# Performance work log

Measured on AMD Instinct MI355X. Metric: run time of the kernel, lower is better.

## Reference

```python
import jax, jax.numpy as jnp
import numpy as np

B, S, F_IN, D, H, L, E, DFF, OUT = 16, 512, 46, 256, 8, 6, 8, 1024, 3


def _ln(x, s, b, eps=1e-5):
    m = x.mean(-1, keepdims=True)
    v = ((x - m) ** 2).mean(-1, keepdims=True)
    return (x - m) / jnp.sqrt(v + eps) * s + b


def _mha(q_in, kv_in, qkv_w, qkv_b, out_w, out_b, h):
    # torch nn.MultiheadAttention (batch_first), eval mode (no dropout)
    d = q_in.shape[-1]
    dh = d // h
    wq, wk, wv = jnp.split(qkv_w, 3, axis=0)
    bq, bk, bv = jnp.split(qkv_b, 3)
    q = (q_in @ wq.T + bq).reshape(q_in.shape[0], q_in.shape[1], h, dh)
    k = (kv_in @ wk.T + bk).reshape(kv_in.shape[0], kv_in.shape[1], h, dh)
    v = (kv_in @ wv.T + bv).reshape(kv_in.shape[0], kv_in.shape[1], h, dh)
    attn = jax.nn.softmax(jnp.einsum('bqhd,bkhd->bhqk', q, k) / jnp.sqrt(jnp.float32(dh)), axis=-1)
    o = jnp.einsum('bhqk,bkhd->bqhd', attn, v).reshape(q_in.shape[0], q_in.shape[1], d)
    return o @ out_w.T + out_b


def _moe(x, gate_w, gate_b, e_w1, e_b1, e_w2, e_b2, top_k=2):
    # Faithful to source: EVERY expert runs its dense FFN over all tokens,
    # then outputs are mixed by the top-k gate weights (zero for unrouted experts).
    logits = x @ gate_w.T + gate_b                      # (B,S,E)
    tk_logits, tk_idx = jax.lax.top_k(logits, top_k)    # (B,S,K)
    tk_probs = jax.nn.softmax(tk_logits, axis=-1)
    onehot = jax.nn.one_hot(tk_idx, logits.shape[-1], dtype=x.dtype)  # (B,S,K,E)
    weights = (onehot * tk_probs[..., None]).sum(-2)    # (B,S,E)
    hid = jax.nn.gelu(jnp.einsum('bsd,efd->bsef', x, e_w1) + e_b1, approximate=False)  # (B,S,E,DFF)
    out_e = jnp.einsum('bsef,edf->bsed', hid, e_w2) + e_b2                             # (B,S,E,D)
    out = jnp.einsum('bsed,bse->bsd', out_e, weights)
    probs = jax.nn.softmax(logits, axis=-1)
    aux = logits.shape[-1] * jnp.sum(probs.mean(axis=(0, 1)) ** 2)
    return out, aux


def _posenc(s, d):
    pos = jnp.arange(s, dtype=jnp.float32)[:, None]
    div = jnp.exp(jnp.arange(0, d, 2, dtype=jnp.float32) * (-np.log(10000.0) / d))
    pe = jnp.zeros((s, d), jnp.float32)
    pe = pe.at[:, 0::2].set(jnp.sin(pos * div)).at[:, 1::2].set(jnp.cos(pos * div))
    return pe


def _forward(x, in_w, in_b, l_qkv_w, l_qkv_b, l_out_w, l_out_b, gate_w, gate_b,
             e_w1, e_b1, e_w2, e_b2, ln1_s, ln1_b, ln2_s, ln2_b,
             p_qkv_w, p_qkv_b, p_out_w, p_out_b,
             a_w1, a_b1, a_ln1s, a_ln1b, a_w2, a_b2, a_ln2s, a_ln2b, a_w3, a_b3,
             pr_w1, pr_b1, pr_ln1s, pr_ln1b, pr_w2, pr_b2, pr_ln2s, pr_ln2b, pr_w3, pr_b3):
    h = x @ in_w.T + in_b + _posenc(x.shape[1], D)[None]
    aux_total = jnp.float32(0.0)
    # NB: source builds ModuleList([encoder_layer]*L) with the SAME instance -> shared weights
    for _ in range(L):
        attn = _mha(h, h, l_qkv_w, l_qkv_b, l_out_w, l_out_b, H)
        h = _ln(h + attn, ln1_s, ln1_b)
        moe_out, aux = _moe(h, gate_w, gate_b, e_w1, e_b1, e_w2, e_b2)
        aux_total = aux_total + aux
        h = _ln(h + moe_out, ln2_s, ln2_b)
    pooled = _mha(h[:, -1:, :], h, p_qkv_w, p_qkv_b, p_out_w, p_out_b, H)[:, 0]  # (B,D)
    # action head: Linear -> GELU -> LN -> Linear -> GELU -> LN -> Linear
    a = jax.nn.gelu(pooled @ a_w1.T + a_b1, approximate=False)
    a = _ln(a, a_ln1s, a_ln1b)
    a = jax.nn.gelu(a @ a_w2.T + a_b2, approximate=False)
    a = _ln(a, a_ln2s, a_ln2b)
    action = a @ a_w3.T + a_b3
    # profit head: Linear -> LN -> GELU -> Linear -> LN -> GELU -> Linear
    p = jax.nn.gelu(_ln(pooled @ pr_w1.T + pr_b1, pr_ln1s, pr_ln1b), approximate=False)
    p = jax.nn.gelu(_ln(p @ pr_w2.T + pr_b2, pr_ln2s, pr_ln2b), approximate=False)
    profit = p @ pr_w3.T + pr_b3
    return action, profit, aux_total


def setup_inputs() -> dict:
    key = jax.random.key(0)
    ks = iter(jax.random.split(key, 64))
    def w(shape, scale=0.02):
        return jax.random.normal(next(ks), shape, jnp.float32) * scale
    d2, d4 = D // 2, D // 4
    return dict(
        x=jax.random.normal(next(ks), (B, S, F_IN), jnp.float32),
        in_w=w((D, F_IN)), in_b=jnp.zeros(D),
        l_qkv_w=w((3 * D, D)), l_qkv_b=jnp.zeros(3 * D), l_out_w=w((D, D)), l_out_b=jnp.zeros(D),
        gate_w=w((E, D)), gate_b=jnp.zeros(E),
        e_w1=w((E, DFF, D)), e_b1=jnp.zeros((E, DFF)), e_w2=w((E, D, DFF)), e_b2=jnp.zeros((E, D)),
        ln1_s=jnp.ones(D), ln1_b=jnp.zeros(D), ln2_s=jnp.ones(D), ln2_b=jnp.zeros(D),
        p_qkv_w=w((3 * D, D)), p_qkv_b=jnp.zeros(3 * D), p_out_w=w((D, D)), p_out_b=jnp.zeros(D),
        a_w1=w((d2, D)), a_b1=jnp.zeros(d2), a_ln1s=jnp.ones(d2), a_ln1b=jnp.zeros(d2),
        a_w2=w((d4, d2)), a_b2=jnp.zeros(d4), a_ln2s=jnp.ones(d4), a_ln2b=jnp.zeros(d4),
        a_w3=w((OUT, d4)), a_b3=jnp.zeros(OUT),
        pr_w1=w((D, D)), pr_b1=jnp.zeros(D), pr_ln1s=jnp.ones(D), pr_ln1b=jnp.zeros(D),
        pr_w2=w((d2, D)), pr_b2=jnp.zeros(d2), pr_ln2s=jnp.ones(d2), pr_ln2b=jnp.zeros(d2),
        pr_w3=w((1, d2)), pr_b3=jnp.zeros(1),
    )


def reference(x, in_w, in_b, l_qkv_w, l_qkv_b, l_out_w, l_out_b, gate_w, gate_b,
              e_w1, e_b1, e_w2, e_b2, ln1_s, ln1_b, ln2_s, ln2_b,
              p_qkv_w, p_qkv_b, p_out_w, p_out_b,
              a_w1, a_b1, a_ln1s, a_ln1b, a_w2, a_b2, a_ln2s, a_ln2b, a_w3, a_b3,
              pr_w1, pr_b1, pr_ln1s, pr_ln1b, pr_w2, pr_b2, pr_ln2s, pr_ln2b, pr_w3, pr_b3):
    return _forward(x, in_w, in_b, l_qkv_w, l_qkv_b, l_out_w, l_out_b, gate_w, gate_b,
                    e_w1, e_b1, e_w2, e_b2, ln1_s, ln1_b, ln2_s, ln2_b,
                    p_qkv_w, p_qkv_b, p_out_w, p_out_b,
                    a_w1, a_b1, a_ln1s, a_ln1b, a_w2, a_b2, a_ln2s, a_ln2b, a_w3, a_b3,
                    pr_w1, pr_b1, pr_ln1s, pr_ln1b, pr_w2, pr_b2, pr_ln2s, pr_ln2b, pr_w3, pr_b3)
```

## Files before the change

### kernel.cpp

```cpp
#include <hip/hip_runtime.h>
#include <hip/hip_bf16.h>
#include <math.h>


typedef __bf16 bf16;
typedef __bf16 bf16x8 __attribute__((ext_vector_type(8)));
typedef __bf16 bf16x4 __attribute__((ext_vector_type(4)));
typedef float f32x4 __attribute__((ext_vector_type(4)));

#define NIN 41

#define GLOAD_LDS(g, l)                                                    \
    __builtin_amdgcn_global_load_lds(                                      \
        (const __attribute__((address_space(1))) void*)(g),                \
        (__attribute__((address_space(3))) void*)(l), 16, 0, 0)

struct InTab {
    const void* src[NIN];
    unsigned off[NIN];
    unsigned n[NIN];
};

__device__ __forceinline__ float gelu_exact(float x) {
    return 0.5f * x * (1.0f + erff(x * 0.70710678118654752f));
}

__device__ __forceinline__ float gelu_fast(float x) {
    const float u = fabsf(x) * 0.70710678118654752f;
    const float t = 1.0f / (1.0f + 0.3275911f * u);
    const float p = t * (0.254829592f + t * (-0.284496736f + t * (1.421413741f +
                    t * (-1.453152027f + t * 1.061405429f))));
    const float er = 1.0f - p * __builtin_exp2f(-u * u * 1.4426950408889634f);
    const float s = (x >= 0.0f) ? er : -er;
    return 0.5f * x * (1.0f + s);
}

__global__ void sniff_kernel(const unsigned* __restrict__ xw, int* __restrict__ flag) {
    __shared__ int cnt;
    if (threadIdx.x == 0) cnt = 0;
    __syncthreads();
    const unsigned w = xw[threadIdx.x];
    const unsigned ex = (w >> 7) & 0xFFu;
    if (ex >= 107u && ex <= 133u) atomicAdd(&cnt, 1);
    __syncthreads();
    if (threadIdx.x == 0) *flag = (cnt >= 192) ? 1 : 0;
}

__global__ __launch_bounds__(256) void convert_kernel(
    InTab tab, bf16* __restrict__ dst_base, const int* __restrict__ flag) {
    const unsigned g0 = blockIdx.x * 1024u;
    int inp = 0;
#pragma unroll
    for (int i = 1; i < NIN; i++)
        if (g0 >= tab.off[i]) inp = i;
    const unsigned n = tab.n[inp];
    const unsigned i0 = g0 - tab.off[inp] + threadIdx.x * 4u;
    if (i0 >= n) return;
    const int isbf = *flag;
    bf16* dst = dst_base + tab.off[inp];
    const unsigned end = (i0 + 4u > n) ? n : i0 + 4u;
    if (isbf) {
        const unsigned short* s = (const unsigned short*)tab.src[inp];
        for (unsigned i = i0; i < end; i++) ((unsigned short*)dst)[i] = s[i];
    } else {
        const float* s = (const float*)tab.src[inp];
        for (unsigned i = i0; i < end; i++) dst[i] = (bf16)s[i];
    }
}

__global__ void out_convert_kernel(const float* __restrict__ st,
                                   const float* __restrict__ auxsums,
                                   void* __restrict__ out,
                                   const int* __restrict__ flag) {
    const int i = threadIdx.x;
    if (i >= 65) return;
    float v;
    if (i == 64) {
        float tot = 0.0f;
        for (int l = 0; l < 6; l++)
            for (int e = 0; e < 8; e++) {
                const float mn = auxsums[l * 8 + e] * (1.0f / 8192.0f);
                tot += 8.0f * mn * mn;
            }
        v = tot;
    } else {
        v = st[i];
    }
    if (*flag) ((bf16*)out)[i] = (bf16)v;
    else       ((float*)out)[i] = v;
}

#define SWZ(r, c) (((r) * 8 + ((c) ^ ((r) & 7))) * 8)

template <int BM, int BN, int WM, int WN, bool VTOUT>
__global__ __launch_bounds__(256) void gemm_bt(
    const bf16* __restrict__ A, const bf16* __restrict__ W,
    const bf16* __restrict__ bias, bf16* __restrict__ C,
    int M, int N, int K, bf16* __restrict__ vT) {
    constexpr int BK = 64;
    __shared__ alignas(16) bf16 smem[BM * BK + BN * BK];
    bf16* As = smem;
    bf16* Ws = smem + BM * BK;
    const int bm0 = blockIdx.x * BM, bn0 = blockIdx.y * BN;
    const int tid = threadIdx.x;
    const int wave = tid >> 6, lane = tid & 63;
    constexpr int WCOLS = BN / WN;
    const int wm0 = (wave / WCOLS) * WM, wn0 = (wave % WCOLS) * WN;
    constexpr int MT = WM / 16, NT = WN / 16;
    f32x4 acc[MT][NT] = {};
    const int frow = lane & 15, fquad = lane >> 4;

    constexpr int AIT = BM / 32, BIT = BN / 32;
    const bf16* ag[AIT];
    const bf16* bg[BIT];
    unsigned al[AIT], bl[BIT];
#pragma unroll
    for (int i = 0; i < AIT; i++) {
        const int d = wave * (BM * 2) + i * 64 + lane;
        const int r = d >> 3, c = ((d & 7) ^ (r & 7)) * 8;
        ag[i] = A + (size_t)(bm0 + r) * K + c;
        al[i] = (unsigned)(wave * (BM * 2) + i * 64) * 8u;
    }
#pragma unroll
    for (int i = 0; i < BIT; i++) {
        const int d = wave * (BN * 2) + i * 64 + lane;
        const int r = d >> 3, c = ((d & 7) ^ (r & 7)) * 8;
        bg[i] = W + (size_t)(bn0 + r) * K + c;
        bl[i] = (unsigned)(wave * (BN * 2) + i * 64) * 8u;
    }

    for (int k0 = 0; k0 < K; k0 += BK) {
#pragma unroll
        for (int i = 0; i < AIT; i++) GLOAD_LDS(ag[i] + k0, &As[al[i]]);
#pragma unroll
        for (int i = 0; i < BIT; i++) GLOAD_LDS(bg[i] + k0, &Ws[bl[i]]);
        __syncthreads();
#pragma unroll
        for (int ks = 0; ks < BK / 32; ks++) {
            bf16x8 af[MT], bfr[NT];
#pragma unroll
            for (int mt = 0; mt < MT; mt++) {
                const int r = wm0 + mt * 16 + frow;
                af[mt] = *(const bf16x8*)&As[SWZ(r, ks * 4 + fquad)];
            }
#pragma unroll
            for (int nt = 0; nt < NT; nt++) {
                const int r = wn0 + nt * 16 + frow;
                bfr[nt] = *(const bf16x8*)&Ws[SWZ(r, ks * 4 + fquad)];
            }
#pragma unroll
            for (int mt = 0; mt < MT; mt++)
#pragma unroll
                for (int nt = 0; nt < NT; nt++)
                    acc[mt][nt] = __builtin_amdgcn_mfma_f32_16x16x32_bf16(
                        af[mt], bfr[nt], acc[mt][nt], 0, 0, 0);
        }
        __syncthreads();
    }

    if (VTOUT && bn0 >= 512) {
#pragma unroll
        for (int mt = 0; mt < MT; mt++)
#pragma unroll
            for (int nt = 0; nt < NT; nt++) {
                const int gn = bn0 + wn0 + nt * 16 + frow;
                const float bv = (float)bias[gn];
                bf16x4 o4;
#pragma unroll
                for (int r = 0; r < 4; r++) o4[r] = (bf16)(acc[mt][nt][r] + bv);
                const int gm0 = bm0 + wm0 + mt * 16 + fquad * 4;
                const int d = gn - 512;
                *(bf16x4*)&vT[((size_t)((gm0 >> 9) * 8 + (d >> 5)) * 32 + (d & 31)) * 512 +
                              (gm0 & 511)] = o4;
            }
    } else {
        bf16* Cs = smem;
#pragma unroll
        for (int mt = 0; mt < MT; mt++)
#pragma unroll
            for (int nt = 0; nt < NT; nt++) {
                const int cl = wn0 + nt * 16 + frow;
                const float bv = (float)bias[bn0 + cl];
#pragma unroll
                for (int r = 0; r < 4; r++)
                    Cs[(wm0 + mt * 16 + fquad * 4 + r) * BN + cl] =
                        (bf16)(acc[mt][nt][r] + bv);
            }
        __syncthreads();
        constexpr int CPR = BN / 8;
        constexpr int CH = (BM * BN) / (256 * 8);
#pragma unroll
        for (int i = 0; i < CH; i++) {
            const int ch = tid + i * 256;
            const int row = ch / CPR;
            const int col = (ch % CPR) * 8;
            *(bf16x8*)&C[(size_t)(bm0 + row) * N + bn0 + col] =
                *(const bf16x8*)&Cs[row * BN + col];
        }
    }
}

__global__ __launch_bounds__(256) void gemm_moe_w1(
    const bf16* __restrict__ A, const bf16* __restrict__ Wb,
    const bf16* __restrict__ biasb, bf16* __restrict__ hid0,
    bf16* __restrict__ hid1, const int* __restrict__ list,
    const int* __restrict__ tile_ex, const int* __restrict__ ntiles) {
    constexpr int BM = 128, BN = 128, BK = 64, WM = 64, WN = 64;
    constexpr int N = 1024, K = 256;
    const int slot = (blockIdx.x >= 71) ? 1 : 0;
    const int xi = blockIdx.x - slot * 71;
    if (xi >= ntiles[slot]) return;
    __shared__ alignas(16) bf16 smem[BM * BK + BN * BK];
    bf16* As = smem;
    bf16* Ws = smem + BM * BK;
    const int* mylist = list + slot * 9216;
    const int e = tile_ex[slot * 72 + xi];
    const bf16* W = Wb + (size_t)e * N * K;
    const bf16* bias = biasb + e * N;
    bf16* C = slot ? hid1 : hid0;
    const int bm0 = xi * BM, bn0 = blockIdx.y * BN;
    const int tid = threadIdx.x;
    const int wave = tid >> 6, lane = tid & 63;
    constexpr int WCOLS = BN / WN;
    const int wm0 = (wave / WCOLS) * WM, wn0 = (wave % WCOLS) * WN;
    constexpr int MT = WM / 16, NT = WN / 16;
    f32x4 acc[MT][NT] = {};
    const int frow = lane & 15, fquad = lane >> 4;

    const bf16* ag[4];
    const bf16* bg[4];
    unsigned al[4], bl[4];
#pragma unroll
    for (int i = 0; i < 4; i++) {
        const int d = wave * 256 + i * 64 + lane;
        const int r = d >> 3, c = ((d & 7) ^ (r & 7)) * 8;
        ag[i] = A + (size_t)mylist[bm0 + r] * K + c;
        al[i] = (unsigned)(wave * 256 + i * 64) * 8u;
        bg[i] = W + (size_t)(bn0 + r) * K + c;
        bl[i] = al[i];
    }

    for (int k0 = 0; k0 < K; k0 += BK) {
#pragma unroll
        for (int i = 0; i < 4; i++) GLOAD_LDS(ag[i] + k0, &As[al[i]]);
#pragma unroll
        for (int i = 0; i < 4; i++) GLOAD_LDS(bg[i] + k0, &Ws[bl[i]]);
        __syncthreads();
#pragma unroll
        for (int ks = 0; ks < 2; ks++) {
            bf16x8 af[MT], bfr[NT];
#pragma unroll
            for (int mt = 0; mt < MT; mt++) {
                const int r = wm0 + mt * 16 + frow;
                af[mt] = *(const bf16x8*)&As[SWZ(r, ks * 4 + fquad)];
            }
#pragma unroll
            for (int nt = 0; nt < NT; nt++) {
                const int r = wn0 + nt * 16 + frow;
                bfr[nt] = *(const bf16x8*)&Ws[SWZ(r, ks * 4 + fquad)];
            }
#pragma unroll
            for (int mt = 0; mt < MT; mt++)
#pragma unroll
                for (int nt = 0; nt < NT; nt++)
                    acc[mt][nt] = __builtin_amdgcn_mfma_f32_16x16x32_bf16(
                        af[mt], bfr[nt], acc[mt][nt], 0, 0, 0);
        }
        __syncthreads();
    }

    {
        bf16* Cs = smem;
#pragma unroll
        for (int mt = 0; mt < MT; mt++)
#pragma unroll
            for (int nt = 0; nt < NT; nt++) {
                const int cl = wn0 + nt * 16 + frow;
                const float bv = (float)bias[bn0 + cl];
#pragma unroll
                for (int r = 0; r < 4; r++)
                    Cs[(wm0 + mt * 16 + fquad * 4 + r) * BN + cl] =
                        (bf16)gelu_fast(acc[mt][nt][r] + bv);
            }
        __syncthreads();
#pragma unroll
        for (int i = 0; i < 8; i++) {
            const int ch = tid + i * 256;
            const int row = ch >> 4;
            const int col = (ch & 15) * 8;
            *(bf16x8*)&C[(size_t)(bm0 + row) * N + bn0 + col] =
                *(const bf16x8*)&Cs[row * BN + col];
        }
    }
}

__global__ __launch_bounds__(256) void gemm_moe_w2(
    const bf16* __restrict__ hid0, const bf16* __restrict__ hid1,
    const bf16* __restrict__ Wb, const bf16* __restrict__ biasb,
    bf16* __restrict__ moe0, bf16* __restrict__ moe1,
    const int* __restrict__ list, const float* __restrict__ lw,
    const int* __restrict__ tile_ex, const int* __restrict__ ntiles) {
    constexpr int BM = 128, BN = 64, BK = 64, WM = 32;
    constexpr int N = 256, K = 1024;
    const int slot = (blockIdx.x >= 71) ? 1 : 0;
    const int xi = blockIdx.x - slot * 71;
    if (xi >= ntiles[slot]) return;
    __shared__ alignas(16) bf16 smem[BM * BK + BN * BK];
    bf16* As = smem;
    bf16* Ws = smem + BM * BK;
    const bf16* A = slot ? hid1 : hid0;
    bf16* C = slot ? moe1 : moe0;
    const int* mylist = list + slot * 9216;
    const float* mylw = lw + slot * 9216;
    const int e = tile_ex[slot * 72 + xi];
    const bf16* W = Wb + (size_t)e * N * K;
    const bf16* bias = biasb + e * N;
    const int bm0 = xi * BM, bn0 = blockIdx.y * BN;
    const int tid = threadIdx.x;
    const int wave = tid >> 6, lane = tid & 63;
    const int wm0 = wave * WM;
    constexpr int MT = WM / 16, NT = 4;
    f32x4 acc[MT][NT] = {};
    const int frow = lane & 15, fquad = lane >> 4;

    const bf16* ag[4];
    const bf16* bg[2];
    unsigned al[4], bl[2];
#pragma unroll
    for (int i = 0; i < 4; i++) {
        const int d = wave * 256 + i * 64 + lane;
        const int r = d >> 3, c = ((d & 7) ^ (r & 7)) * 8;
        ag[i] = A + (size_t)(bm0 + r) * K + c;
        al[i] = (unsigned)(wave * 256 + i * 64) * 8u;
    }
#pragma unroll
    for (int i = 0; i < 2; i++) {
        const int d = wave * 128 + i * 64 + lane;
        const int r = d >> 3, c = ((d & 7) ^ (r & 7)) * 8;
        bg[i] = W + (size_t)(bn0 + r) * K + c;
        bl[i] = (unsigned)(wave * 128 + i * 64) * 8u;
    }

    for (int k0 = 0; k0 < K; k0 += BK) {
#pragma unroll
        for (int i = 0; i < 4; i++) GLOAD_LDS(ag[i] + k0, &As[al[i]]);
#pragma unroll
        for (int i = 0; i < 2; i++) GLOAD_LDS(bg[i] + k0, &Ws[bl[i]]);
        __syncthreads();
#pragma unroll
        for (int ks = 0; ks < 2; ks++) {
            bf16x8 af[MT], bfr[NT];
#pragma unroll
            for (int mt = 0; mt < MT; mt++) {
                const int r = wm0 + mt * 16 + frow;
                af[mt] = *(const bf16x8*)&As[SWZ(r, ks * 4 + fquad)];
            }
#pragma unroll
            for (int nt = 0; nt < NT; nt++) {
                const int r = nt * 16 + frow;
                bfr[nt] = *(const bf16x8*)&Ws[SWZ(r, ks * 4 + fquad)];
            }
#pragma unroll
            for (int mt = 0; mt < MT; mt++)
#pragma unroll
                for (int nt = 0; nt < NT; nt++)
                    acc[mt][nt] = __builtin_amdgcn_mfma_f32_16x16x32_bf16(
                        af[mt], bfr[nt], acc[mt][nt], 0, 0, 0);
        }
        __syncthreads();
    }

    {
        bf16* Cs = smem;
        float lwv[MT][4];
#pragma unroll
        for (int mt = 0; mt < MT; mt++)
#pragma unroll
            for (int r = 0; r < 4; r++)
                lwv[mt][r] = mylw[bm0 + wm0 + mt * 16 + fquad * 4 + r];
#pragma unroll
        for (int mt = 0; mt < MT; mt++)
#pragma unroll
            for (int nt = 0; nt < NT; nt++) {
                const int cl = nt * 16 + frow;
                const float bv = (float)bias[bn0 + cl];
#pragma unroll
                for (int r = 0; r < 4; r++)
                    Cs[(wm0 + mt * 16 + fquad * 4 + r) * BN + cl] =
                        (bf16)(lwv[mt][r] * (acc[mt][nt][r] + bv));
            }
        __syncthreads();
#pragma unroll
        for (int i = 0; i < 4; i++) {
            const int ch = tid + i * 256;
            const int row = ch >> 3;
            const int col = (ch & 7) * 8;
            *(bf16x8*)&C[(size_t)mylist[bm0 + row] * 256 + bn0 + col] =
                *(const bf16x8*)&Cs[row * BN + col];
        }
    }
}

__global__ __launch_bounds__(256) void input_proj_kernel(
    const bf16* __restrict__ x, const bf16* __restrict__ w,
    const bf16* __restrict__ b, bf16* __restrict__ h) {
    const int m = blockIdx.x, t = threadIdx.x;
    __shared__ float xs[46];
    if (t < 46) xs[t] = (float)x[m * 46 + t];
    __syncthreads();
    float acc = (float)b[t];
#pragma unroll
    for (int k = 0; k < 46; k++) acc += xs[k] * (float)w[t * 46 + k];
    const int s = m & 511;
    const int i = t >> 1;
    const float dv = expf((float)(2 * i) * (-9.210340371976184f / 256.0f));
    const float ang = (float)s * dv;
    const float pe = (t & 1) ? cosf(ang) : sinf(ang);
    h[(size_t)m * 256 + t] = (bf16)(acc + pe);
}

__global__ __launch_bounds__(256) void ln_kernel(
    bf16* __restrict__ h, const bf16* __restrict__ a0,
    const bf16* __restrict__ a1, const bf16* __restrict__ s,
    const bf16* __restrict__ b) {
    const int wv = threadIdx.x >> 6, lane = threadIdx.x & 63;
    const int m = blockIdx.x * 8 + wv * 2 + (lane >> 5);
    const int c0 = (lane & 31) * 8;
    const size_t off = (size_t)m * 256 + c0;
    bf16x8 hv = *(const bf16x8*)&h[off];
    bf16x8 av = *(const bf16x8*)&a0[off];
    bf16x8 bv2 = *(const bf16x8*)&a1[off];
    float x[8];
    float s1 = 0.0f, s2 = 0.0f;
#pragma unroll
    for (int j = 0; j < 8; j++) {
        x[j] = (float)hv[j] + (float)av[j] + (float)bv2[j];
        s1 += x[j];
        s2 += x[j] * x[j];
    }
#pragma unroll
    for (int msk = 1; msk < 32; msk <<= 1) {
        s1 += __shfl_xor(s1, msk, 64);
        s2 += __shfl_xor(s2, msk, 64);
    }
    const float mean = s1 * (1.0f / 256.0f);
    const float var = fmaxf(s2 * (1.0f / 256.0f) - mean * mean, 0.0f);
    const float inv = rsqrtf(var + 1e-5f);
    bf16x8 sv = *(const bf16x8*)&s[c0];
    bf16x8 bv = *(const bf16x8*)&b[c0];
    bf16x8 o;
#pragma unroll
    for (int j = 0; j < 8; j++)
        o[j] = (bf16)((x[j] - mean) * inv * (float)sv[j] + (float)bv[j]);
    *(bf16x8*)&h[off] = o;
}

__global__ __launch_bounds__(256) void proj_gate_ln_kernel(
    const bf16* __restrict__ A, const bf16* __restrict__ W,
    const bf16* __restrict__ bias, bf16* __restrict__ h,
    const bf16* __restrict__ lns, const bf16* __restrict__ lnb,
    const bf16* __restrict__ gw, const bf16* __restrict__ gb,
    int* __restrict__ top_e, float* __restrict__ top_w,
    int* __restrict__ g_hist, float* __restrict__ aux_sums) {
    __shared__ alignas(16) bf16 As[32 * 64];
    __shared__ alignas(16) bf16 Ws[256 * 64];
    __shared__ alignas(16) bf16 hs[32 * 264];
    __shared__ alignas(16) bf16 gws[8 * 264];
    __shared__ float rws1[4][32], rws2[4][32];
    __shared__ float meanv[32], invv[32];
    __shared__ float lg[256];
    __shared__ int sh_hist[16];
    __shared__ float sh_aux[8];

    const int bm0 = blockIdx.x * 32;
    const int tid = threadIdx.x;
    const int wave = tid >> 6, lane = tid & 63;
    const int wn0 = (wave & 3) * 64;
    const int frow = lane & 15, fquad = lane >> 4;
    f32x4 acc[2][4] = {};

    const int da = wave * 64 + lane;
// ... 429 lines not shown
        for (int k = 0; k < 256; k += 8) {
            bf16x8 wv = *(const bf16x8*)&wr[k];
#pragma unroll
            for (int q = 0; q < 8; q++) a += pool[k + q] * (float)wv[q];
        }
        buf[t] = gelu_exact(a);
    }
    __syncthreads();
    block_ln(buf, 128, aln1s, aln1b);
    if (t < 64) {
        float a = (float)ab2[t];
        const bf16* wr = &aw2[t * 128];
        for (int k = 0; k < 128; k += 8) {
            bf16x8 wv = *(const bf16x8*)&wr[k];
#pragma unroll
            for (int q = 0; q < 8; q++) a += buf[k + q] * (float)wv[q];
        }
        buf2[t] = gelu_exact(a);
    }
    __syncthreads();
    block_ln(buf2, 64, aln2s, aln2b);
    if (t < 3) {
        float a = (float)ab3[t];
        for (int k = 0; k < 64; k++) a += buf2[k] * (float)aw3[t * 64 + k];
        out[b * 3 + t] = a;
    }

    {
        float a = (float)pb1[t];
        const bf16* wr = &pw1[t * 256];
        for (int k = 0; k < 256; k += 8) {
            bf16x8 wv = *(const bf16x8*)&wr[k];
#pragma unroll
            for (int q = 0; q < 8; q++) a += pool[k + q] * (float)wv[q];
        }
        buf[t] = a;
    }
    __syncthreads();
    block_ln(buf, 256, pln1s, pln1b);
    buf[t] = gelu_exact(buf[t]);
    __syncthreads();
    if (t < 128) {
        float a = (float)pb2[t];
        const bf16* wr = &pw2[t * 256];
        for (int k = 0; k < 256; k += 8) {
            bf16x8 wv = *(const bf16x8*)&wr[k];
#pragma unroll
            for (int q = 0; q < 8; q++) a += buf[k + q] * (float)wv[q];
        }
        buf2[t] = a;
    }
    __syncthreads();
    block_ln(buf2, 128, pln2s, pln2b);
    if (t < 128) buf2[t] = gelu_exact(buf2[t]);
    __syncthreads();
    if (t == 0) {
        float a = (float)pb3[0];
        for (int k = 0; k < 128; k++) a += buf2[k] * (float)pw3[k];
        out[48 + b] = a;
    }
}

extern "C" void kernel_launch(void* const* d_in, const int* in_sizes, int n_in,
                              void* d_out, int out_size, void* d_ws, size_t ws_size,
                              hipStream_t stream) {
    char* ws = (char*)d_ws;
    const size_t MB = 1024 * 1024;
    bf16*  h     = (bf16*)(ws);
    bf16*  moe0  = (bf16*)(ws + 8 * MB);
    bf16*  moe1  = (bf16*)(ws + 13 * MB);
    char*  ctrl  = ws + 20 * MB;
    float* auxs   = (float*)(ctrl + 0);
    int*   flag   = (int*)(ctrl + 192);
    int*   ntiles = (int*)(ctrl + 256);
    int*   tileex = (int*)(ctrl + 320);
    float* ostage = (float*)(ctrl + 1024);
    int*   g_hist = (int*)(ctrl + 2048);
    int*   top_e  = (int*)(ctrl + 20480);
    float* top_w  = (float*)(ctrl + 86016);
    int*   list   = (int*)(ctrl + 151552);
    float* lw     = (float*)(ctrl + 225280);
    bf16*  qkv   = (bf16*)(ws + 24 * MB);
    bf16*  aoutb = (bf16*)(ws + 40 * MB);
    bf16*  hid0  = (bf16*)(ws + 56 * MB);
    bf16*  hid1  = (bf16*)(ws + 80 * MB);
    bf16*  vT    = (bf16*)(ws + 104 * MB);
    float* pattn = (float*)(ws + 110 * MB);
    bf16*  cvbase = (bf16*)(ws + 112 * MB);

    InTab tab;
    unsigned off = 0;
    bf16* cv[NIN];
    for (int i = 0; i < NIN; i++) {
        tab.src[i] = d_in[i];
        tab.off[i] = off;
        tab.n[i] = (unsigned)in_sizes[i];
        cv[i] = cvbase + off;
        off += ((unsigned)in_sizes[i] + 1023u) & ~1023u;
    }
    const int cv_blocks = (int)(off >> 10);

    const bf16 *x = cv[0], *in_w = cv[1], *in_b = cv[2], *qkv_w = cv[3], *qkv_b = cv[4],
               *out_w = cv[5], *out_b = cv[6], *gate_w = cv[7], *gate_b = cv[8],
               *e_w1 = cv[9], *e_b1 = cv[10], *e_w2 = cv[11], *e_b2 = cv[12],
               *ln1_s = cv[13], *ln1_b = cv[14], *ln2_s = cv[15], *ln2_b = cv[16],
               *pqkv_w = cv[17], *pqkv_b = cv[18], *pout_w = cv[19], *pout_b = cv[20],
               *a_w1 = cv[21], *a_b1 = cv[22], *a_ln1s = cv[23], *a_ln1b = cv[24],
               *a_w2 = cv[25], *a_b2 = cv[26], *a_ln2s = cv[27], *a_ln2b = cv[28],
               *a_w3 = cv[29], *a_b3 = cv[30],
               *pr_w1 = cv[31], *pr_b1 = cv[32], *pr_ln1s = cv[33], *pr_ln1b = cv[34],
               *pr_w2 = cv[35], *pr_b2 = cv[36], *pr_ln2s = cv[37], *pr_ln2b = cv[38],
               *pr_w3 = cv[39], *pr_b3 = cv[40];

    sniff_kernel<<<1, 256, 0, stream>>>((const unsigned*)d_in[0], flag);
    convert_kernel<<<cv_blocks, 256, 0, stream>>>(tab, cvbase, flag);

    hipMemsetAsync(auxs, 0, 192, stream);
    input_proj_kernel<<<8192, 256, 0, stream>>>(x, in_w, in_b, h);

    for (int l = 0; l < 6; l++) {
        gemm_bt<64, 128, 32, 64, true><<<dim3(128, 6), 256, 0, stream>>>(
            h, qkv_w, qkv_b, qkv, 8192, 768, 256, vT);
        attn_kernel<<<dim3(16, 128), 256, 0, stream>>>(qkv, vT, aoutb);
        proj_gate_ln_kernel<<<256, 256, 0, stream>>>(
            aoutb, out_w, out_b, h, ln1_s, ln1_b, gate_w, gate_b,
            top_e, top_w, g_hist, auxs + l * 8);
        scatter_route_kernel<<<64, 256, 0, stream>>>(g_hist, top_e, top_w,
                                                     ntiles, tileex, list, lw);
        gemm_moe_w1<<<dim3(142, 8), 256, 0, stream>>>(
            h, e_w1, e_b1, hid0, hid1, list, tileex, ntiles);
        gemm_moe_w2<<<dim3(142, 4), 256, 0, stream>>>(
            hid0, hid1, e_w2, e_b2, moe0, moe1, list, lw, tileex, ntiles);
        ln_kernel<<<1024, 256, 0, stream>>>(h, moe0, moe1, ln2_s, ln2_b);
    }

    gemm_bt<64, 128, 32, 64, true><<<dim3(128, 6), 256, 0, stream>>>(
        h, pqkv_w, pqkv_b, qkv, 8192, 768, 256, vT);
    pooled_attn_kernel<<<128, 256, 0, stream>>>(qkv, vT, pattn);
    heads_kernel<<<16, 256, 0, stream>>>(
        pattn, pout_w, pout_b,
        a_w1, a_b1, a_ln1s, a_ln1b, a_w2, a_b2, a_ln2s, a_ln2b, a_w3, a_b3,
        pr_w1, pr_b1, pr_ln1s, pr_ln1b, pr_w2, pr_b2, pr_ln2s, pr_ln2b, pr_w3, pr_b3,
        ostage);
    out_convert_kernel<<<1, 128, 0, stream>>>(ostage, auxs, d_out, flag);
}
```

Measured before the change: 1.007 ms.

## Fuse MoE expert W1+GELU and W2 GEMMs into one kernel keeping hidden in LDS

Replaces the two routed-expert GEMM kernels with a single fused kernel. Each block takes 32 routed tokens, computes the hidden activations in 256-column chunks into shared memory, and immediately accumulates the second GEMM. This avoids writing and re-reading the large hidden tensor through global memory and drops one launch. The cost is smaller M tiles with low per-block reuse of expert weights, each block re-reading the full W1/W2 for its expert, and no load/compute overlap. It also zeroes a padding row after h, presumably to cover a sentinel index in the gather lists.

```diff
diff --git a/kernel.cpp b/kernel.cpp
--- a/kernel.cpp
+++ b/kernel.cpp
@@ -91,6 +91,7 @@
 }
 
 #define SWZ(r, c) (((r) * 8 + ((c) ^ ((r) & 7))) * 8)
+#define SWZ256(r, c) (((r) * 32 + ((c) ^ ((r) & 7))) * 8)
 
 template <int BM, int BN, int WM, int WN, bool VTOUT>
 __global__ __launch_bounds__(256) void gemm_bt(
@@ -200,203 +201,147 @@
     }
 }
 
-__global__ __launch_bounds__(256) void gemm_moe_w1(
-    const bf16* __restrict__ A, const bf16* __restrict__ Wb,
-    const bf16* __restrict__ biasb, bf16* __restrict__ hid0,
-    bf16* __restrict__ hid1, const int* __restrict__ list,
-    const int* __restrict__ tile_ex, const int* __restrict__ ntiles) {
-    constexpr int BM = 128, BN = 128, BK = 64, WM = 64, WN = 64;
-    constexpr int N = 1024, K = 256;
-    const int slot = (blockIdx.x >= 71) ? 1 : 0;
-    const int xi = blockIdx.x - slot * 71;
-    if (xi >= ntiles[slot]) return;
-    __shared__ alignas(16) bf16 smem[BM * BK + BN * BK];
-    bf16* As = smem;
-    bf16* Ws = smem + BM * BK;
+__global__ __launch_bounds__(256) void gemm_moe_fused(
+    const bf16* __restrict__ hsrc, const bf16* __restrict__ W1b,
+    const bf16* __restrict__ b1b, const bf16* __restrict__ W2b,
+    const bf16* __restrict__ b2b, bf16* __restrict__ moe0,
+    bf16* __restrict__ moe1, const int* __restrict__ list,
+    const float* __restrict__ lw, const int* __restrict__ tile_ex,
+    const int* __restrict__ ntiles) {
+    __shared__ alignas(16) bf16 As[32 * 256];
+    __shared__ alignas(16) bf16 Hs[32 * 256];
+    __shared__ alignas(16) bf16 Ws[256 * 64];
+    const int slot = (blockIdx.x >= 284) ? 1 : 0;
+    const int xi = (int)blockIdx.x - slot * 284;
+    if (xi >= (ntiles[slot] << 2)) return;
     const int* mylist = list + slot * 9216;
-    const int e = tile_ex[slot * 72 + xi];
-    const bf16* W = Wb + (size_t)e * N * K;
-    const bf16* bias = biasb + e * N;
-    bf16* C = slot ? hid1 : hid0;
-    const int bm0 = xi * BM, bn0 = blockIdx.y * BN;
-    const int tid = threadIdx.x;
-    const int wave = tid >> 6, lane = tid & 63;
-    constexpr int WCOLS = BN / WN;
-    const int wm0 = (wave / WCOLS) * WM, wn0 = (wave % WCOLS) * WN;
-    constexpr int MT = WM / 16, NT = WN / 16;
-    f32x4 acc[MT][NT] = {};
+    const float* mylw = lw + slot * 9216;
+    const int e = tile_ex[slot * 72 + (xi >> 2)];
+    const bf16* W1 = W1b + (size_t)e * 1024 * 256;
+    const bf16* b1 = b1b + e * 1024;
+    const bf16* W2 = W2b + (size_t)e * 256 * 1024;
+    const bf16* b2 = b2b + e * 256;
+    bf16* C = slot ? moe1 : moe0;
+    const int bm0 = xi * 32;
+    const int tid = threadIdx.x, wave = tid >> 6, lane = tid & 63;
     const int frow = lane & 15, fquad = lane >> 4;
-
-    const bf16* ag[4];
-    const bf16* bg[4];
-    unsigned al[4], bl[4];
+    const int wn0 = wave * 64;
+
 #pragma unroll
     for (int i = 0; i < 4; i++) {
         const int d = wave * 256 + i * 64 + lane;
-        const int r = d >> 3, c = ((d & 7) ^ (r & 7)) * 8;
-        ag[i] = A + (size_t)mylist[bm0 + r] * K + c;
-        al[i] = (unsigned)(wave * 256 + i * 64) * 8u;
-        bg[i] = W + (size_t)(bn0 + r) * K + c;
-        bl[i] = al[i];
-    }
-
-    for (int k0 = 0; k0 < K; k0 += BK) {
-#pragma unroll
-        for (int i = 0; i < 4; i++) GLOAD_LDS(ag[i] + k0, &As[al[i]]);
-#pragma unroll
-        for (int i = 0; i < 4; i++) GLOAD_LDS(bg[i] + k0, &Ws[bl[i]]);
-        __syncthreads();
-#pragma unroll
-        for (int ks = 0; ks < 2; ks++) {
-            bf16x8 af[MT], bfr[NT];
-#pragma unroll
-            for (int mt = 0; mt < MT; mt++) {
-                const int r = wm0 + mt * 16 + frow;
-                af[mt] = *(const bf16x8*)&As[SWZ(r, ks * 4 + fquad)];
-            }
-#pragma unroll
-            for (int nt = 0; nt < NT; nt++) {
-                const int r = wn0 + nt * 16 + frow;
-                bfr[nt] = *(const bf16x8*)&Ws[SWZ(r, ks * 4 + fquad)];
-            }
-#pragma unroll
-            for (int mt = 0; mt < MT; mt++)
-#pragma unroll
-                for (int nt = 0; nt < NT; nt++)
-                    acc[mt][nt] = __builtin_amdgcn_mfma_f32_16x16x32_bf16(
-                        af[mt], bfr[nt], acc[mt][nt], 0, 0, 0);
-        }
-        __syncthreads();
+        const int r = d >> 5, c = ((d & 31) ^ (r & 7)) * 8;
+        GLOAD_LDS(hsrc + (size_t)mylist[bm0 + r] * 256 + c, &As[d * 8]);
+    }
+
+    f32x4 macc[2][4] = {};
+#pragma unroll 1
+    for (int nc = 0; nc < 4; nc++) {
+        f32x4 acc1[2][4] = {};
+        for (int k0 = 0; k0 < 256; k0 += 64) {
+#pragma unroll
+            for (int i = 0; i < 8; i++) {
+                const int d = wave * 512 + i * 64 + lane;
+                const int r = d >> 3, c = ((d & 7) ^ (r & 7)) * 8;
+                GLOAD_LDS(W1 + (size_t)(nc * 256 + r) * 256 + k0 + c, &Ws[d * 8]);
+            }
+            __syncthreads();
+#pragma unroll
+            for (int ks = 0; ks < 2; ks++) {
+                bf16x8 af[2], bfr[4];
+#pragma unroll
+                for (int mt = 0; mt < 2; mt++) {
+                    const int r = mt * 16 + frow;
+                    const int kc = (k0 >> 3) + ks * 4 + fquad;
+                    af[mt] = *(const bf16x8*)&As[SWZ256(r, kc)];
+                }
+#pragma unroll
+                for (int nt = 0; nt < 4; nt++) {
+                    const int r = wn0 + nt * 16 + frow;
+                    bfr[nt] = *(const bf16x8*)&Ws[SWZ(r, ks * 4 + fquad)];
+                }
+#pragma unroll
+                for (int mt = 0; mt < 2; mt++)
+#pragma unroll
+                    for (int nt = 0; nt < 4; nt++)
+                        acc1[mt][nt] = __builtin_amdgcn_mfma_f32_16x16x32_bf16(
+                            af[mt], bfr[nt], acc1[mt][nt], 0, 0, 0);
+            }
+            __syncthreads();
+        }
+#pragma unroll
+        for (int mt = 0; mt < 2; mt++)
+#pragma unroll
+            for (int nt = 0; nt < 4; nt++) {
+                const int gn = wn0 + nt * 16 + frow;
+                const float bv = (float)b1[nc * 256 + gn];
+#pragma unroll
+                for (int r = 0; r < 4; r++) {
+                    const int gm = mt * 16 + fquad * 4 + r;
+                    Hs[SWZ256(gm, gn >> 3) + (gn & 7)] =
+                        (bf16)gelu_fast(acc1[mt][nt][r] + bv);
+                }
+            }
+        __syncthreads();
+        for (int k0 = 0; k0 < 256; k0 += 64) {
+#pragma unroll
+            for (int i = 0; i < 8; i++) {
+                const int d = wave * 512 + i * 64 + lane;
+                const int r = d >> 3, c = ((d & 7) ^ (r & 7)) * 8;
+                GLOAD_LDS(W2 + (size_t)r * 1024 + nc * 256 + k0 + c, &Ws[d * 8]);
+            }
+            __syncthreads();
+#pragma unroll
+            for (int ks = 0; ks < 2; ks++) {
+                bf16x8 af[2], bfr[4];
+#pragma unroll
+                for (int mt = 0; mt < 2; mt++) {
+                    const int r = mt * 16 + frow;
+                    const int kc = (k0 >> 3) + ks * 4 + fquad;
+                    af[mt] = *(const bf16x8*)&Hs[SWZ256(r, kc)];
+                }
+#pragma unroll
+                for (int nt = 0; nt < 4; nt++) {
+                    const int r = wn0 + nt * 16 + frow;
+                    bfr[nt] = *(const bf16x8*)&Ws[SWZ(r, ks * 4 + fquad)];
+                }
+#pragma unroll
+                for (int mt = 0; mt < 2; mt++)
+#pragma unroll
+                    for (int nt = 0; nt < 4; nt++)
+                        macc[mt][nt] = __builtin_amdgcn_mfma_f32_16x16x32_bf16(
+                            af[mt], bfr[nt], macc[mt][nt], 0, 0, 0);
+            }
+            __syncthreads();
+        }
     }
 
     {
-        bf16* Cs = smem;
-#pragma unroll
-        for (int mt = 0; mt < MT; mt++)
-#pragma unroll
-            for (int nt = 0; nt < NT; nt++) {
-                const int cl = wn0 + nt * 16 + frow;
-                const float bv = (float)bias[bn0 + cl];
-#pragma unroll
-                for (int r = 0; r < 4; r++)
-                    Cs[(wm0 + mt * 16 + fquad * 4 + r) * BN + cl] =
-                        (bf16)gelu_fast(acc[mt][nt][r] + bv);
-            }
-        __syncthreads();
-#pragma unroll
-        for (int i = 0; i < 8; i++) {
-            const int ch = tid + i * 256;
-            const int row = ch >> 4;
-            const int col = (ch & 15) * 8;
-            *(bf16x8*)&C[(size_t)(bm0 + row) * N + bn0 + col] =
-                *(const bf16x8*)&Cs[row * BN + col];
-        }
-    }
-}
-
-__global__ __launch_bounds__(256) void gemm_moe_w2(
-    const bf16* __restrict__ hid0, const bf16* __restrict__ hid1,
-    const bf16* __restrict__ Wb, const bf16* __restrict__ biasb,
-    bf16* __restrict__ moe0, bf16* __restrict__ moe1,
-    const int* __restrict__ list, const float* __restrict__ lw,
-    const int* __restrict__ tile_ex, const int* __restrict__ ntiles) {
-    constexpr int BM = 128, BN = 64, BK = 64, WM = 32;
-    constexpr int N = 256, K = 1024;
-    const int slot = (blockIdx.x >= 71) ? 1 : 0;
-    const int xi = blockIdx.x - slot * 71;
-    if (xi >= ntiles[slot]) return;
-    __shared__ alignas(16) bf16 smem[BM * BK + BN * BK];
-    bf16* As = smem;
-    bf16* Ws = smem + BM * BK;
-    const bf16* A = slot ? hid1 : hid0;
-    bf16* C = slot ? moe1 : moe0;
-    const int* mylist = list + slot * 9216;
-    const float* mylw = lw + slot * 9216;
-    const int e = tile_ex[slot * 72 + xi];
-    const bf16* W = Wb + (size_t)e * N * K;
-    const bf16* bias = biasb + e * N;
-    const int bm0 = xi * BM, bn0 = blockIdx.y * BN;
-    const int tid = threadIdx.x;
-    const int wave = tid >> 6, lane = tid & 63;
-    const int wm0 = wave * WM;
-    constexpr int MT = WM / 16, NT = 4;
-    f32x4 acc[MT][NT] = {};
-    const int frow = lane & 15, fquad = lane >> 4;
-
-    const bf16* ag[4];
-    const bf16* bg[2];
-    unsigned al[4], bl[2];
-#pragma unroll
-    for (int i = 0; i < 4; i++) {
-        const int d = wave * 256 + i * 64 + lane;
-        const int r = d >> 3, c = ((d & 7) ^ (r & 7)) * 8;
-        ag[i] = A + (size_t)(bm0 + r) * K + c;
-        al[i] = (unsigned)(wave * 256 + i * 64) * 8u;
-    }
-#pragma unroll
-    for (int i = 0; i < 2; i++) {
-        const int d = wave * 128 + i * 64 + lane;
-        const int r = d >> 3, c = ((d & 7) ^ (r & 7)) * 8;
-        bg[i] = W + (size_t)(bn0 + r) * K + c;
-        bl[i] = (unsigned)(wave * 128 + i * 64) * 8u;
-    }
-
-    for (int k0 = 0; k0 < K; k0 += BK) {
-#pragma unroll
-        for (int i = 0; i < 4; i++) GLOAD_LDS(ag[i] + k0, &As[al[i]]);
-#pragma unroll
-        for (int i = 0; i < 2; i++) GLOAD_LDS(bg[i] + k0, &Ws[bl[i]]);
-        __syncthreads();
-#pragma unroll
-        for (int ks = 0; ks < 2; ks++) {
-            bf16x8 af[MT], bfr[NT];
-#pragma unroll
-            for (int mt = 0; mt < MT; mt++) {
-                const int r = wm0 + mt * 16 + frow;
-                af[mt] = *(const bf16x8*)&As[SWZ(r, ks * 4 + fquad)];
-            }
-#pragma unroll
-            for (int nt = 0; nt < NT; nt++) {
-                const int r = nt * 16 + frow;
-                bfr[nt] = *(const bf16x8*)&Ws[SWZ(r, ks * 4 + fquad)];
-            }
-#pragma unroll
-            for (int mt = 0; mt < MT; mt++)
-#pragma unroll
-                for (int nt = 0; nt < NT; nt++)
-                    acc[mt][nt] = __builtin_amdgcn_mfma_f32_16x16x32_bf16(
-                        af[mt], bfr[nt], acc[mt][nt], 0, 0, 0);
-        }
-        __syncthreads();
-    }
-
-    {
-        bf16* Cs = smem;
-        float lwv[MT][4];
-#pragma unroll
-        for (int mt = 0; mt < MT; mt++)
+        float lwv[2][4];
+#pragma unroll
+        for (int mt = 0; mt < 2; mt++)
 #pragma unroll
             for (int r = 0; r < 4; r++)
-                lwv[mt][r] = mylw[bm0 + wm0 + mt * 16 + fquad * 4 + r];
-#pragma unroll
-        for (int mt = 0; mt < MT; mt++)
-#pragma unroll
-            for (int nt = 0; nt < NT; nt++) {
-                const int cl = nt * 16 + frow;
-                const float bv = (float)bias[bn0 + cl];
-#pragma unroll
-                for (int r = 0; r < 4; r++)
-                    Cs[(wm0 + mt * 16 + fquad * 4 + r) * BN + cl] =
-                        (bf16)(lwv[mt][r] * (acc[mt][nt][r] + bv));
+                lwv[mt][r] = mylw[bm0 + mt * 16 + fquad * 4 + r];
+#pragma unroll
+        for (int mt = 0; mt < 2; mt++)
+#pragma unroll
+            for (int nt = 0; nt < 4; nt++) {
+                const int gn = wn0 + nt * 16 + frow;
+                const float bv = (float)b2[gn];
+#pragma unroll
+                for (int r = 0; r < 4; r++) {
+                    const int gm = mt * 16 + fquad * 4 + r;
+                    As[gm * 256 + gn] = (bf16)(lwv[mt][r] * (macc[mt][nt][r] + bv));
+                }
             }
         __syncthreads();
 #pragma unroll
         for (int i = 0; i < 4; i++) {
             const int ch = tid + i * 256;
-            const int row = ch >> 3;
-            const int col = (ch & 7) * 8;
-            *(bf16x8*)&C[(size_t)mylist[bm0 + row] * 256 + bn0 + col] =
-                *(const bf16x8*)&Cs[row * BN + col];
+            const int row = ch >> 5, col = (ch & 31) * 8;
+            *(bf16x8*)&C[(size_t)mylist[bm0 + row] * 256 + col] =
+                *(const bf16x8*)&As[row * 256 + col];
         }
     }
 }
@@ -992,8 +937,6 @@
     float* lw     = (float*)(ctrl + 225280);
     bf16*  qkv   = (bf16*)(ws + 24 * MB);
     bf16*  aoutb = (bf16*)(ws + 40 * MB);
-    bf16*  hid0  = (bf16*)(ws + 56 * MB);
-    bf16*  hid1  = (bf16*)(ws + 80 * MB);
     bf16*  vT    = (bf16*)(ws + 104 * MB);
     float* pattn = (float*)(ws + 110 * MB);
     bf16*  cvbase = (bf16*)(ws + 112 * MB);
@@ -1026,6 +969,7 @@
     convert_kernel<<<cv_blocks, 256, 0, stream>>>(tab, cvbase, flag);
 
     hipMemsetAsync(auxs, 0, 192, stream);
+    hipMemsetAsync((char*)h + (size_t)8192 * 512, 0, 512, stream);
     input_proj_kernel<<<8192, 256, 0, stream>>>(x, in_w, in_b, h);
 
     for (int l = 0; l < 6; l++) {
@@ -1037,10 +981,8 @@
             top_e, top_w, g_hist, auxs + l * 8);
         scatter_route_kernel<<<64, 256, 0, stream>>>(g_hist, top_e, top_w,
                                                      ntiles, tileex, list, lw);
-        gemm_moe_w1<<<dim3(142, 8), 256, 0, stream>>>(
-            h, e_w1, e_b1, hid0, hid1, list, tileex, ntiles);
-        gemm_moe_w2<<<dim3(142, 4), 256, 0, stream>>>(
-            hid0, hid1, e_w2, e_b2, moe0, moe1, list, lw, tileex, ntiles);
+        gemm_moe_fused<<<568, 256, 0, stream>>>(
+            h, e_w1, e_b1, e_w2, e_b2, moe0, moe1, list, lw, tileex, ntiles);
         ln_kernel<<<1024, 256, 0, stream>>>(h, moe0, moe1, ln2_s, ln2_b);
     }
 
```

Result: slower. 1.126 ms (+11.9%).

## Double-buffer LDS staging in MoE expert GEMMs to overlap loads with MFMA

Applied to the files above, without the earlier changes.

Both MoE expert GEMM kernels now use two LDS buffers per operand. The next K-slice is issued with global_load_lds before the current slice is computed, and explicit vmcnt waits plus raw barriers replace __syncthreads. The goal is to hide global-to-LDS latency behind the MFMA work instead of stalling every iteration. In exchange, shared-memory use per block doubles, which may lower occupancy, and correctness depends on the hand-set vmcnt counts matching the number of outstanding loads.

```diff
diff --git a/kernel.cpp b/kernel.cpp
--- a/kernel.cpp
+++ b/kernel.cpp
@@ -210,9 +210,8 @@
     const int slot = (blockIdx.x >= 71) ? 1 : 0;
     const int xi = blockIdx.x - slot * 71;
     if (xi >= ntiles[slot]) return;
-    __shared__ alignas(16) bf16 smem[BM * BK + BN * BK];
-    bf16* As = smem;
-    bf16* Ws = smem + BM * BK;
+    __shared__ alignas(16) bf16 As[2][BM * BK];
+    __shared__ alignas(16) bf16 Ws[2][BN * BK];
     const int* mylist = list + slot * 9216;
     const int e = tile_ex[slot * 72 + xi];
     const bf16* W = Wb + (size_t)e * N * K;
@@ -240,24 +239,36 @@
         bl[i] = al[i];
     }
 
+    auto stage = [&](int buf, int k0) {
+#pragma unroll
+        for (int i = 0; i < 4; i++) GLOAD_LDS(ag[i] + k0, &As[buf][al[i]]);
+#pragma unroll
+        for (int i = 0; i < 4; i++) GLOAD_LDS(bg[i] + k0, &Ws[buf][bl[i]]);
+    };
+
+    stage(0, 0);
+    int cur = 0;
     for (int k0 = 0; k0 < K; k0 += BK) {
-#pragma unroll
-        for (int i = 0; i < 4; i++) GLOAD_LDS(ag[i] + k0, &As[al[i]]);
-#pragma unroll
-        for (int i = 0; i < 4; i++) GLOAD_LDS(bg[i] + k0, &Ws[bl[i]]);
-        __syncthreads();
+        if (k0 + BK < K) {
+            stage(cur ^ 1, k0 + BK);
+            asm volatile("s_waitcnt vmcnt(8)" ::: "memory");
+        } else {
+            asm volatile("s_waitcnt vmcnt(0)" ::: "memory");
+        }
+        __builtin_amdgcn_s_barrier();
+        __builtin_amdgcn_sched_barrier(0);
 #pragma unroll
         for (int ks = 0; ks < 2; ks++) {
             bf16x8 af[MT], bfr[NT];
 #pragma unroll
             for (int mt = 0; mt < MT; mt++) {
                 const int r = wm0 + mt * 16 + frow;
-                af[mt] = *(const bf16x8*)&As[SWZ(r, ks * 4 + fquad)];
+                af[mt] = *(const bf16x8*)&As[cur][SWZ(r, ks * 4 + fquad)];
             }
 #pragma unroll
             for (int nt = 0; nt < NT; nt++) {
                 const int r = wn0 + nt * 16 + frow;
-                bfr[nt] = *(const bf16x8*)&Ws[SWZ(r, ks * 4 + fquad)];
+                bfr[nt] = *(const bf16x8*)&Ws[cur][SWZ(r, ks * 4 + fquad)];
             }
 #pragma unroll
             for (int mt = 0; mt < MT; mt++)
@@ -266,11 +277,13 @@
                     acc[mt][nt] = __builtin_amdgcn_mfma_f32_16x16x32_bf16(
                         af[mt], bfr[nt], acc[mt][nt], 0, 0, 0);
         }
-        __syncthreads();
+        __builtin_amdgcn_sched_barrier(0);
+        __builtin_amdgcn_s_barrier();
+        cur ^= 1;
     }
 
     {
-        bf16* Cs = smem;
+        bf16* Cs = &As[0][0];
 #pragma unroll
         for (int mt = 0; mt < MT; mt++)
 #pragma unroll
@@ -305,9 +318,8 @@
     const int slot = (blockIdx.x >= 71) ? 1 : 0;
     const int xi = blockIdx.x - slot * 71;
     if (xi >= ntiles[slot]) return;
-    __shared__ alignas(16) bf16 smem[BM * BK + BN * BK];
-    bf16* As = smem;
-    bf16* Ws = smem + BM * BK;
+    __shared__ alignas(16) bf16 As[2][BM * BK];
+    __shared__ alignas(16) bf16 Ws[2][BN * BK];
     const bf16* A = slot ? hid1 : hid0;
     bf16* C = slot ? moe1 : moe0;
     const int* mylist = list + slot * 9216;
@@ -341,24 +353,36 @@
         bl[i] = (unsigned)(wave * 128 + i * 64) * 8u;
     }
 
+    auto stage = [&](int buf, int k0) {
+#pragma unroll
+        for (int i = 0; i < 4; i++) GLOAD_LDS(ag[i] + k0, &As[buf][al[i]]);
+#pragma unroll
+        for (int i = 0; i < 2; i++) GLOAD_LDS(bg[i] + k0, &Ws[buf][bl[i]]);
+    };
+
+    stage(0, 0);
+    int cur = 0;
     for (int k0 = 0; k0 < K; k0 += BK) {
-#pragma unroll
-        for (int i = 0; i < 4; i++) GLOAD_LDS(ag[i] + k0, &As[al[i]]);
-#pragma unroll
-        for (int i = 0; i < 2; i++) GLOAD_LDS(bg[i] + k0, &Ws[bl[i]]);
-        __syncthreads();
+        if (k0 + BK < K) {
+            stage(cur ^ 1, k0 + BK);
+            asm volatile("s_waitcnt vmcnt(6)" ::: "memory");
+        } else {
+            asm volatile("s_waitcnt vmcnt(0)" ::: "memory");
+        }
+        __builtin_amdgcn_s_barrier();
+        __builtin_amdgcn_sched_barrier(0);
 #pragma unroll
         for (int ks = 0; ks < 2; ks++) {
             bf16x8 af[MT], bfr[NT];
 #pragma unroll
             for (int mt = 0; mt < MT; mt++) {
                 const int r = wm0 + mt * 16 + frow;
-                af[mt] = *(const bf16x8*)&As[SWZ(r, ks * 4 + fquad)];
+                af[mt] = *(const bf16x8*)&As[cur][SWZ(r, ks * 4 + fquad)];
             }
 #pragma unroll
             for (int nt = 0; nt < NT; nt++) {
                 const int r = nt * 16 + frow;
-                bfr[nt] = *(const bf16x8*)&Ws[SWZ(r, ks * 4 + fquad)];
+                bfr[nt] = *(const bf16x8*)&Ws[cur][SWZ(r, ks * 4 + fquad)];
             }
 #pragma unroll
             for (int mt = 0; mt < MT; mt++)
@@ -367,11 +391,13 @@
                     acc[mt][nt] = __builtin_amdgcn_mfma_f32_16x16x32_bf16(
                         af[mt], bfr[nt], acc[mt][nt], 0, 0, 0);
         }
-        __syncthreads();
+        __builtin_amdgcn_sched_barrier(0);
+        __builtin_amdgcn_s_barrier();
+        cur ^= 1;
     }
 
     {
-        bf16* Cs = smem;
+        bf16* Cs = &As[0][0];
         float lwv[MT][4];
 #pragma unroll
         for (int mt = 0; mt < MT; mt++)
```

Result: slower. 1.044 ms (+3.7%).

## Keep gathered MoE A-tile resident in LDS and loop over all N chunks

Applied to the files above, without the earlier changes.

The MoE first-layer GEMM now loads a 64-row gathered token tile with full K=256 into LDS once, then iterates over all eight 128-column output chunks inside one block, streaming only the expert weights. This removes the repeated indirect gather of token rows that happened once per N-block in the old 2D grid. In exchange the grid shrinks to 284 blocks with a serial loop over N chunks, using less parallelism and more LDS per block. A memset of a padding row past h is added, presumably so gathers of padded list entries read zeros.

```diff
diff --git a/kernel.cpp b/kernel.cpp
--- a/kernel.cpp
+++ b/kernel.cpp
@@ -91,6 +91,7 @@
 }
 
 #define SWZ(r, c) (((r) * 8 + ((c) ^ ((r) & 7))) * 8)
+#define SWZ256(r, c) (((r) * 32 + ((c) ^ ((r) & 7))) * 8)
 
 template <int BM, int BN, int WM, int WN, bool VTOUT>
 __global__ __launch_bounds__(256) void gemm_bt(
@@ -201,95 +202,89 @@
 }
 
 __global__ __launch_bounds__(256) void gemm_moe_w1(
-    const bf16* __restrict__ A, const bf16* __restrict__ Wb,
+    const bf16* __restrict__ Asrc, const bf16* __restrict__ Wb,
     const bf16* __restrict__ biasb, bf16* __restrict__ hid0,
     bf16* __restrict__ hid1, const int* __restrict__ list,
     const int* __restrict__ tile_ex, const int* __restrict__ ntiles) {
-    constexpr int BM = 128, BN = 128, BK = 64, WM = 64, WN = 64;
     constexpr int N = 1024, K = 256;
-    const int slot = (blockIdx.x >= 71) ? 1 : 0;
-    const int xi = blockIdx.x - slot * 71;
-    if (xi >= ntiles[slot]) return;
-    __shared__ alignas(16) bf16 smem[BM * BK + BN * BK];
-    bf16* As = smem;
-    bf16* Ws = smem + BM * BK;
+    __shared__ alignas(16) bf16 As[64 * 256];
+    __shared__ alignas(16) bf16 Ws[128 * 64];
+    const int slot = (blockIdx.x >= 142) ? 1 : 0;
+    const int xi = (int)blockIdx.x - slot * 142;
+    if (xi >= (ntiles[slot] << 1)) return;
     const int* mylist = list + slot * 9216;
-    const int e = tile_ex[slot * 72 + xi];
+    const int e = tile_ex[slot * 72 + (xi >> 1)];
     const bf16* W = Wb + (size_t)e * N * K;
     const bf16* bias = biasb + e * N;
     bf16* C = slot ? hid1 : hid0;
-    const int bm0 = xi * BM, bn0 = blockIdx.y * BN;
-    const int tid = threadIdx.x;
-    const int wave = tid >> 6, lane = tid & 63;
-    constexpr int WCOLS = BN / WN;
-    const int wm0 = (wave / WCOLS) * WM, wn0 = (wave % WCOLS) * WN;
-    constexpr int MT = WM / 16, NT = WN / 16;
-    f32x4 acc[MT][NT] = {};
+    const int bm0 = xi * 64;
+    const int tid = threadIdx.x, wave = tid >> 6, lane = tid & 63;
     const int frow = lane & 15, fquad = lane >> 4;
-
-    const bf16* ag[4];
-    const bf16* bg[4];
-    unsigned al[4], bl[4];
-#pragma unroll
-    for (int i = 0; i < 4; i++) {
-        const int d = wave * 256 + i * 64 + lane;
-        const int r = d >> 3, c = ((d & 7) ^ (r & 7)) * 8;
-        ag[i] = A + (size_t)mylist[bm0 + r] * K + c;
-        al[i] = (unsigned)(wave * 256 + i * 64) * 8u;
-        bg[i] = W + (size_t)(bn0 + r) * K + c;
-        bl[i] = al[i];
-    }
-
-    for (int k0 = 0; k0 < K; k0 += BK) {
-#pragma unroll
-        for (int i = 0; i < 4; i++) GLOAD_LDS(ag[i] + k0, &As[al[i]]);
-#pragma unroll
-        for (int i = 0; i < 4; i++) GLOAD_LDS(bg[i] + k0, &Ws[bl[i]]);
-        __syncthreads();
-#pragma unroll
-        for (int ks = 0; ks < 2; ks++) {
-            bf16x8 af[MT], bfr[NT];
-#pragma unroll
-            for (int mt = 0; mt < MT; mt++) {
-                const int r = wm0 + mt * 16 + frow;
-                af[mt] = *(const bf16x8*)&As[SWZ(r, ks * 4 + fquad)];
-            }
-#pragma unroll
-            for (int nt = 0; nt < NT; nt++) {
-                const int r = wn0 + nt * 16 + frow;
-                bfr[nt] = *(const bf16x8*)&Ws[SWZ(r, ks * 4 + fquad)];
-            }
-#pragma unroll
-            for (int mt = 0; mt < MT; mt++)
-#pragma unroll
-                for (int nt = 0; nt < NT; nt++)
-                    acc[mt][nt] = __builtin_amdgcn_mfma_f32_16x16x32_bf16(
-                        af[mt], bfr[nt], acc[mt][nt], 0, 0, 0);
-        }
-        __syncthreads();
-    }
-
-    {
-        bf16* Cs = smem;
-#pragma unroll
-        for (int mt = 0; mt < MT; mt++)
-#pragma unroll
-            for (int nt = 0; nt < NT; nt++) {
-                const int cl = wn0 + nt * 16 + frow;
-                const float bv = (float)bias[bn0 + cl];
-#pragma unroll
-                for (int r = 0; r < 4; r++)
-                    Cs[(wm0 + mt * 16 + fquad * 4 + r) * BN + cl] =
-                        (bf16)gelu_fast(acc[mt][nt][r] + bv);
-            }
-        __syncthreads();
-#pragma unroll
-        for (int i = 0; i < 8; i++) {
-            const int ch = tid + i * 256;
-            const int row = ch >> 4;
-            const int col = (ch & 15) * 8;
-            *(bf16x8*)&C[(size_t)(bm0 + row) * N + bn0 + col] =
-                *(const bf16x8*)&Cs[row * BN + col];
+    const int wm0 = (wave >> 1) * 32, wn0 = (wave & 1) * 64;
+
+#pragma unroll
+    for (int i = 0; i < 8; i++) {
+        const int d = wave * 512 + i * 64 + lane;
+        const int r = d >> 5, cc = (d & 31) ^ (r & 7);
+        GLOAD_LDS(Asrc + (size_t)mylist[bm0 + r] * 256 + cc * 8, &As[d * 8]);
+    }
+
+#pragma unroll 1
+    for (int nc = 0; nc < 8; nc++) {
+        f32x4 acc[2][4] = {};
+        for (int k0 = 0; k0 < 256; k0 += 64) {
+#pragma unroll
+            for (int i = 0; i < 4; i++) {
+                const int d = wave * 256 + i * 64 + lane;
+                const int r = d >> 3, c = ((d & 7) ^ (r & 7)) * 8;
+                GLOAD_LDS(W + (size_t)(nc * 128 + r) * 256 + k0 + c, &Ws[d * 8]);
+            }
+            __syncthreads();
+#pragma unroll
+            for (int ks = 0; ks < 2; ks++) {
+                bf16x8 af[2], bfr[4];
+#pragma unroll
+                for (int mt = 0; mt < 2; mt++) {
+                    const int r = wm0 + mt * 16 + frow;
+                    const int kc = (k0 >> 3) + ks * 4 + fquad;
+                    af[mt] = *(const bf16x8*)&As[SWZ256(r, kc)];
+                }
+#pragma unroll
+                for (int nt = 0; nt < 4; nt++) {
+                    const int r = wn0 + nt * 16 + frow;
+                    bfr[nt] = *(const bf16x8*)&Ws[SWZ(r, ks * 4 + fquad)];
+                }
+#pragma unroll
+                for (int mt = 0; mt < 2; mt++)
+#pragma unroll
+                    for (int nt = 0; nt < 4; nt++)
+                        acc[mt][nt] = __builtin_amdgcn_mfma_f32_16x16x32_bf16(
+                            af[mt], bfr[nt], acc[mt][nt], 0, 0, 0);
+            }
+            __syncthreads();
+        }
+        {
+            bf16* Cs = Ws;
+#pragma unroll
+            for (int mt = 0; mt < 2; mt++)
+#pragma unroll
+                for (int nt = 0; nt < 4; nt++) {
+                    const int cl = wn0 + nt * 16 + frow;
+                    const float bv = (float)bias[nc * 128 + cl];
+#pragma unroll
+                    for (int r = 0; r < 4; r++)
+                        Cs[(wm0 + mt * 16 + fquad * 4 + r) * 128 + cl] =
+                            (bf16)gelu_fast(acc[mt][nt][r] + bv);
+                }
+            __syncthreads();
+#pragma unroll
+            for (int i = 0; i < 4; i++) {
+                const int ch = tid + i * 256;
+                const int row = ch >> 4, col = (ch & 15) * 8;
+                *(bf16x8*)&C[(size_t)(bm0 + row) * N + nc * 128 + col] =
+                    *(const bf16x8*)&Cs[row * 128 + col];
+            }
+            __syncthreads();
         }
     }
 }
@@ -1026,6 +1021,7 @@
     convert_kernel<<<cv_blocks, 256, 0, stream>>>(tab, cvbase, flag);
 
     hipMemsetAsync(auxs, 0, 192, stream);
+    hipMemsetAsync((char*)h + (size_t)8192 * 512, 0, 512, stream);
     input_proj_kernel<<<8192, 256, 0, stream>>>(x, in_w, in_b, h);
 
     for (int l = 0; l < 6; l++) {
@@ -1037,7 +1033,7 @@
             top_e, top_w, g_hist, auxs + l * 8);
         scatter_route_kernel<<<64, 256, 0, stream>>>(g_hist, top_e, top_w,
                                                      ntiles, tileex, list, lw);
-        gemm_moe_w1<<<dim3(142, 8), 256, 0, stream>>>(
+        gemm_moe_w1<<<284, 256, 0, stream>>>(
             h, e_w1, e_b1, hid0, hid1, list, tileex, ntiles);
         gemm_moe_w2<<<dim3(142, 4), 256, 0, stream>>>(
             hid0, hid1, e_w2, e_b2, moe0, moe1, list, lw, tileex, ntiles);
```

After: 1.212 ms. 20.4% more time.
